# Kernel tuning notes

Hardware: AMD Instinct MI355X
Metric: run time of the kernel (lower is better)

## Reference

```python
import jax, jax.numpy as jnp
import numpy as np

HEADS = 8
DIM_HEAD = 64
SCALE = DIM_HEAD ** -0.5


def setup_inputs() -> dict:
    key = jax.random.key(0)
    ks = jax.random.split(key, 7)
    B, Nq, Nc = 4, 2048, 2048
    Dq, Dc = 1024, 768
    inner = HEADS * DIM_HEAD  # 512
    x = jax.random.normal(ks[0], (B, Nq, Dq), dtype=jnp.float32)
    context = jax.random.normal(ks[1], (B, Nc, Dc), dtype=jnp.float32)
    # Linear weights stored as (in, out) so y = x @ W, matching torch Linear math.
    Wq = jax.random.normal(ks[2], (Dq, inner), dtype=jnp.float32) * (Dq ** -0.5)
    Wk = jax.random.normal(ks[3], (Dc, inner), dtype=jnp.float32) * (Dc ** -0.5)
    Wv = jax.random.normal(ks[4], (Dc, inner), dtype=jnp.float32) * (Dc ** -0.5)
    Wo = jax.random.normal(ks[5], (inner, Dq), dtype=jnp.float32) * (inner ** -0.5)
    bo = jax.random.normal(ks[6], (Dq,), dtype=jnp.float32) * 0.01
    return {"x": x, "context": context, "Wq": Wq, "Wk": Wk, "Wv": Wv, "Wo": Wo, "bo": bo}


def reference(x, context, Wq, Wk, Wv, Wo, bo):
    B, Nq, _ = x.shape
    # projections -> [b, n, h, d]
    q = (x @ Wq).reshape(B, Nq, HEADS, DIM_HEAD)
    k = (context @ Wk).reshape(B, context.shape[1], HEADS, DIM_HEAD)
    v = (context @ Wv).reshape(B, context.shape[1], HEADS, DIM_HEAD)
    # scores [b, h, i, j]
    sim = jnp.einsum('bihd,bjhd->bhij', q, k) * SCALE
    attn = jax.nn.softmax(sim, axis=-1)
    out = jnp.einsum('bhij,bjhd->bihd', attn, v)  # [b, i, h, d]
    out = out.reshape(B, Nq, HEADS * DIM_HEAD)
    return out @ Wo + bo
```

## Files before the change

kernel.cpp:

```cpp
#include <hip/hip_runtime.h>
#include <hip/hip_bf16.h>


typedef __bf16 bf16_8 __attribute__((ext_vector_type(8)));
typedef __bf16 bf16_4 __attribute__((ext_vector_type(4)));
typedef float f32_4 __attribute__((ext_vector_type(4)));
typedef float f32_16 __attribute__((ext_vector_type(16)));
typedef int i32x2 __attribute__((ext_vector_type(2)));
typedef int i32x4 __attribute__((ext_vector_type(4)));

#define AS1 __attribute__((address_space(1)))
#define AS3 __attribute__((address_space(3)))

__device__ __forceinline__ void gld_lds16(const __bf16* g, __bf16* l) {
  __builtin_amdgcn_global_load_lds((AS1 unsigned int*)(void*)g,
                                   (AS3 unsigned int*)(void*)l, 16, 0, 0);
}

__device__ __forceinline__ void lds_fence() {
  __asm__ volatile("" ::: "memory");
  __builtin_amdgcn_s_waitcnt(0xC07F);
  __asm__ volatile("" ::: "memory");
}

__device__ __forceinline__ int cvt_pk(float lo, float hi) {
  int r;
  __asm__("v_cvt_pk_bf16_f32 %0, %1, %2" : "=v"(r) : "v"(lo), "v"(hi));
  return r;
}

__global__ __launch_bounds__(256) void prep(
    const float* __restrict__ x, const float* __restrict__ ctx,
    const float* __restrict__ Wq, const float* __restrict__ Wk,
    const float* __restrict__ Wv, const float* __restrict__ Wo,
    __bf16* __restrict__ xb, __bf16* __restrict__ ctxb,
    __bf16* __restrict__ WqT, __bf16* __restrict__ WkT,
    __bf16* __restrict__ WvT, __bf16* __restrict__ WoT) {
  int tb = blockIdx.x;
  if (tb >= 1792) {
    tb -= 1792;
    const float* src;
    __bf16* dst;
    size_t base;
    if (tb < 4096) { src = x; dst = xb; base = (size_t)tb * 2048; }
    else { src = ctx; dst = ctxb; base = (size_t)(tb - 4096) * 2048; }
    const size_t idx = base + threadIdx.x * 8;
    const f32_4 f0 = *(const f32_4*)(src + idx);
    const f32_4 f1 = *(const f32_4*)(src + idx + 4);
    bf16_8 v;
#pragma unroll
    for (int i = 0; i < 4; ++i) { v[i] = (__bf16)f0[i]; v[4 + i] = (__bf16)f1[i]; }
    *(bf16_8*)(dst + idx) = v;
    return;
  }
  __shared__ __bf16 t[32][33];
  const float* W; __bf16* Wt; int K, N;
  if (tb < 512)       { W = Wq; Wt = WqT; K = 1024; N = 512; }
  else if (tb < 896)  { tb -= 512;  W = Wk; Wt = WkT; K = 768; N = 512; }
  else if (tb < 1280) { tb -= 896;  W = Wv; Wt = WvT; K = 768; N = 512; }
  else                { tb -= 1280; W = Wo; Wt = WoT; K = 512; N = 1024; }
  const int nx = N >> 5;
  const int n0 = (tb % nx) * 32, k0 = (tb / nx) * 32;
  const int tx = threadIdx.x & 31, ty = threadIdx.x >> 5;
#pragma unroll
  for (int r = 0; r < 32; r += 8)
    t[ty + r][tx] = (__bf16)W[(size_t)(k0 + ty + r) * N + n0 + tx];
  __syncthreads();
#pragma unroll
  for (int r = 0; r < 32; r += 8)
    Wt[(size_t)(n0 + ty + r) * K + k0 + tx] = t[tx][ty + r];
}

__global__ __launch_bounds__(256, 2) void proj(
    const __bf16* __restrict__ xb, const __bf16* __restrict__ ctxb,
    const __bf16* __restrict__ WqT, const __bf16* __restrict__ WkvT,
    __bf16* __restrict__ Qb, __bf16* __restrict__ Kbuf,
    __bf16* __restrict__ Vtb) {
  __shared__ __align__(16) __bf16 As[2][128 * 64];
  __shared__ __align__(16) __bf16 Bs[2][128 * 64];
  int tb = blockIdx.x;
  const __bf16 *A, *Bt;
  int K, bm, bn, mode;
  if (tb < 256) {
    A = xb; Bt = WqT; K = 1024; mode = 0;
    bn = (tb & 3) << 7; bm = (tb >> 2) << 7;
  } else {
    tb -= 256;
    A = ctxb; Bt = WkvT; K = 768; mode = 1;
    bn = (tb & 7) << 7; bm = (tb >> 3) << 7;
  }
  const int tid = threadIdx.x;
  const int lane = tid & 63;
  const int wave = tid >> 6;
  const int wi = (wave >> 1) * 64;
  const int wn = (wave & 1) * 64;
  const int lrow = lane & 15;
  const int quad = lane >> 4;
  const int lkey = lrow & 7;
  const int srow = tid >> 3;
  const int scol = (tid & 7) * 8;
  const int swz = (((scol >> 3) ^ (srow & 7)) * 8);

  f32_4 acc[4][4];
#pragma unroll
  for (int i = 0; i < 4; ++i)
#pragma unroll
    for (int j = 0; j < 4; ++j)
#pragma unroll
      for (int r = 0; r < 4; ++r) acc[i][j][r] = 0.0f;

  auto stage = [&](int buf, int kt) {
#pragma unroll
    for (int r = 0; r < 4; ++r) {
      const int row = r * 32 + srow;
      gld_lds16(A + (size_t)(bm + row) * K + kt + swz, &As[buf][row * 64 + scol]);
    }
#pragma unroll
    for (int r = 0; r < 4; ++r) {
      const int row = r * 32 + srow;
      gld_lds16(Bt + (size_t)(bn + row) * K + kt + swz, &Bs[buf][row * 64 + scol]);
    }
  };

  stage(0, 0);
  const int nkt = K >> 6;
  for (int kti = 0; kti < nkt; ++kti) {
    __syncthreads();
    if (kti + 1 < nkt) stage((kti + 1) & 1, (kti + 1) * 64);
    const __bf16* Asb = As[kti & 1];
    const __bf16* Bsb = Bs[kti & 1];
#pragma unroll
    for (int ks = 0; ks < 2; ++ks) {
      bf16_8 af[4], bfv[4];
#pragma unroll
      for (int t = 0; t < 4; ++t)
        af[t] = *(const bf16_8*)(Asb + (wi + t * 16 + lrow) * 64 +
                                 (((ks * 4 + quad) ^ lkey) * 8));
#pragma unroll
      for (int t = 0; t < 4; ++t)
        bfv[t] = *(const bf16_8*)(Bsb + (wn + t * 16 + lrow) * 64 +
                                  (((ks * 4 + quad) ^ lkey) * 8));
#pragma unroll
      for (int it = 0; it < 4; ++it)
#pragma unroll
        for (int nt = 0; nt < 4; ++nt)
          acc[it][nt] = __builtin_amdgcn_mfma_f32_16x16x32_bf16(
              af[it], bfv[nt], acc[it][nt], 0, 0, 0);
    }
  }

#pragma unroll
  for (int nt = 0; nt < 4; ++nt) {
    const int c = bn + wn + nt * 16 + lrow;
    if (mode == 0) {
#pragma unroll
      for (int it = 0; it < 4; ++it) {
        const int rbase = bm + wi + it * 16 + quad * 4;
#pragma unroll
        for (int r = 0; r < 4; ++r)
          Qb[(size_t)(rbase + r) * 512 + c] = (__bf16)(acc[it][nt][r] * 0.125f);
      }
    } else if (c < 512) {
#pragma unroll
      for (int it = 0; it < 4; ++it) {
        const int rbase = bm + wi + it * 16 + quad * 4;
#pragma unroll
        for (int r = 0; r < 4; ++r)
          Kbuf[(size_t)(rbase + r) * 512 + c] = (__bf16)acc[it][nt][r];
      }
    } else {
      const int vcol = c - 512;
      const int bhh = ((bm >> 11) << 3) + (vcol >> 6);
      const int d = vcol & 63;
#pragma unroll
      for (int it = 0; it < 4; ++it) {
        const int jb = (bm & 2047) + wi + it * 16 + quad * 4;
        bf16_4 pk;
#pragma unroll
        for (int r = 0; r < 4; ++r) pk[r] = (__bf16)acc[it][nt][r];
        *(bf16_4*)&Vtb[((size_t)(bhh * 64 + d)) * 2048 + jb] = pk;
      }
    }
  }
}

__global__ __launch_bounds__(256, 3) void attn_fwd(const __bf16* __restrict__ Q,
                                                   const __bf16* __restrict__ Kb,
                                                   const __bf16* __restrict__ Vt,
                                                   __bf16* __restrict__ AO) {
  __shared__ __align__(16) __bf16 Ks[2][64 * 64];
  __shared__ __align__(16) __bf16 Vs[2][64 * 64];
  __shared__ __align__(16) float Ls[4][32];
  const int tid = threadIdx.x;
  const int lane = tid & 63;
  const int wave = tid >> 6;
  const int did = blockIdx.x;
  const int sid = did >> 3;
  const int bh = ((did & 7) << 2) + (sid & 3);
  const int ib = sid >> 2;
  const int b = bh >> 3, h = bh & 7;
  const int i0 = ib * 128 + wave * 32;
  const int li = lane & 31;
  const int hi = lane >> 5;
  const int key = li & 7;
  const size_t bq = (size_t)b * 2048;
  const int hc = h * 64;

  const int ssub = lane >> 3;
  const int sch = lane & 7;
  const int sswz = (sch ^ ssub) * 8;

  const __bf16* Kg = Kb + bq * 512 + hc;
  const __bf16* Vg = Vt + (size_t)bh * 64 * 2048;

  auto stage = [&](int buf, int j0) {
#pragma unroll
    for (int t = 0; t < 2; ++t) {
      const int rb = wave * 16 + t * 8;
      gld_lds16(Kg + (size_t)(j0 + rb + ssub) * 512 + sswz, &Ks[buf][rb * 64]);
      gld_lds16(Vg + (size_t)(rb + ssub) * 2048 + j0 + sswz, &Vs[buf][rb * 64]);
    }
  };

  bf16_8 aq[4];
#pragma unroll
  for (int ks = 0; ks < 4; ++ks)
    aq[ks] = *(const bf16_8*)(Q + (bq + i0 + li) * 512 + hc + ks * 16 + hi * 8);

  float psl = 0.0f;
  f32_16 oacc[2];
#pragma unroll
  for (int d = 0; d < 2; ++d)
#pragma unroll
    for (int r = 0; r < 16; ++r) oacc[d][r] = 0.0f;

  stage(0, 0);

  for (int jt = 0; jt < 32; ++jt) {
    __syncthreads();
    if (jt + 1 < 32) stage((jt + 1) & 1, (jt + 1) * 64);
    const __bf16* Ksb = Ks[jt & 1];
    const __bf16* Vsb = Vs[jt & 1];

    f32_16 sacc[2];
#pragma unroll
    for (int jb = 0; jb < 2; ++jb)
#pragma unroll
      for (int r = 0; r < 16; ++r) sacc[jb][r] = 0.0f;
    __builtin_amdgcn_s_setprio(1);
#pragma unroll
    for (int jb = 0; jb < 2; ++jb) {
#pragma unroll
      for (int ks = 0; ks < 4; ++ks) {
        const bf16_8 ak = *(const bf16_8*)(
            Ksb + (jb * 32 + li) * 64 + (((ks * 2 + hi) ^ key) * 8));
        sacc[jb] = __builtin_amdgcn_mfma_f32_32x32x16_bf16(
            ak, aq[ks], sacc[jb], 0, 0, 0);
      }
    }
    __builtin_amdgcn_s_setprio(0);

    int pw[4][4];
#pragma unroll
    for (int jb = 0; jb < 2; ++jb) {
      float p[16];
#pragma unroll
      for (int r = 0; r < 16; ++r) p[r] = __expf(sacc[jb][r]);
      float s0 = 0.0f, s1 = 0.0f;
#pragma unroll
      for (int r = 0; r < 8; ++r) { s0 += p[2 * r]; s1 += p[2 * r + 1]; }
      psl += s0 + s1;
      const int c01 = cvt_pk(p[0], p[1]),   c23 = cvt_pk(p[2], p[3]);
      const int c45 = cvt_pk(p[4], p[5]),   c67 = cvt_pk(p[6], p[7]);
      const int c89 = cvt_pk(p[8], p[9]),   cab = cvt_pk(p[10], p[11]);
      const int ccd = cvt_pk(p[12], p[13]), cef = cvt_pk(p[14], p[15]);
      const i32x2 r02 = __builtin_amdgcn_permlane32_swap(c01, c45, false, false);
      const i32x2 r13 = __builtin_amdgcn_permlane32_swap(c23, c67, false, false);
      const i32x2 r46 = __builtin_amdgcn_permlane32_swap(c89, ccd, false, false);
      const i32x2 r57 = __builtin_amdgcn_permlane32_swap(cab, cef, false, false);
      pw[jb * 2][0] = r02[0];     pw[jb * 2][1] = r13[0];
      pw[jb * 2][2] = r02[1];     pw[jb * 2][3] = r13[1];
      pw[jb * 2 + 1][0] = r46[0]; pw[jb * 2 + 1][1] = r57[0];
      pw[jb * 2 + 1][2] = r46[1]; pw[jb * 2 + 1][3] = r57[1];
    }

    __builtin_amdgcn_s_setprio(1);
#pragma unroll
    for (int ks2 = 0; ks2 < 4; ++ks2) {
      i32x4 w4;
      w4[0] = pw[ks2][0]; w4[1] = pw[ks2][1];
      w4[2] = pw[ks2][2]; w4[3] = pw[ks2][3];
      const bf16_8 ap = __builtin_bit_cast(bf16_8, w4);
#pragma unroll
      for (int dblk = 0; dblk < 2; ++dblk) {
        const bf16_8 bv = *(const bf16_8*)(
            Vsb + (dblk * 32 + li) * 64 + (((ks2 * 2 + hi) ^ key) * 8));
        oacc[dblk] = __builtin_amdgcn_mfma_f32_32x32x16_bf16(
            ap, bv, oacc[dblk], 0, 0, 0);
      }
    }
    __builtin_amdgcn_s_setprio(0);
  }

  const float tot = psl + __shfl_xor(psl, 32);
  const float inv = 1.0f / tot;
  if (lane < 32) Ls[wave][li] = inv;
  lds_fence();
  f32_4 ic[4];
#pragma unroll
  for (int g = 0; g < 4; ++g)
    ic[g] = *(const f32_4*)(&Ls[wave][8 * g + 4 * hi]);

#pragma unroll
  for (int dblk = 0; dblk < 2; ++dblk)
#pragma unroll
    for (int g = 0; g < 4; ++g)
#pragma unroll
      for (int r = 0; r < 4; ++r) {
        const size_t rg = bq + i0 + 8 * g + 4 * hi + r;
        AO[rg * 512 + hc + dblk * 32 + li] =
            (__bf16)(oacc[dblk][4 * g + r] * ic[g][r]);
      }
}

__global__ __launch_bounds__(256, 2) void gemm_out(const __bf16* __restrict__ A,
                                                   const __bf16* __restrict__ Bt,
                                                   float* __restrict__ C,
                                                   const float* __restrict__ bias) {
  __shared__ __align__(16) __bf16 As[2][128 * 64];
  __shared__ __align__(16) __bf16 Bs[2][128 * 64];
  const int K = 512, N = 1024;
  const int tid = threadIdx.x;
  const int lane = tid & 63;
  const int wave = tid >> 6;
  const int wi = (wave >> 1) * 64;
  const int wn = (wave & 1) * 64;
  const int bm = blockIdx.y * 128;
  const int bn = blockIdx.x * 128;
  const int lrow = lane & 15;
  const int quad = lane >> 4;
  const int lkey = lrow & 7;
  const int srow = tid >> 3;
  const int scol = (tid & 7) * 8;
  const int swz = (((scol >> 3) ^ (srow & 7)) * 8);

  f32_4 acc[4][4];
#pragma unroll
  for (int i = 0; i < 4; ++i)
#pragma unroll
    for (int j = 0; j < 4; ++j)
#pragma unroll
      for (int r = 0; r < 4; ++r) acc[i][j][r] = 0.0f;

  auto stage = [&](int buf, int kt) {
#pragma unroll
    for (int r = 0; r < 4; ++r) {
      const int row = r * 32 + srow;
      gld_lds16(A + (size_t)(bm + row) * K + kt + swz, &As[buf][row * 64 + scol]);
      gld_lds16(Bt + (size_t)(bn + row) * K + kt + swz, &Bs[buf][row * 64 + scol]);
    }
  };

  stage(0, 0);
  for (int kti = 0; kti < 8; ++kti) {
    __syncthreads();
    if (kti + 1 < 8) stage((kti + 1) & 1, (kti + 1) * 64);
    const __bf16* Asb = As[kti & 1];
    const __bf16* Bsb = Bs[kti & 1];
#pragma unroll
    for (int ks = 0; ks < 2; ++ks) {
      bf16_8 af[4], bfv[4];
#pragma unroll
      for (int t = 0; t < 4; ++t)
        af[t] = *(const bf16_8*)(Asb + (wi + t * 16 + lrow) * 64 +
                                 (((ks * 4 + quad) ^ lkey) * 8));
#pragma unroll
      for (int t = 0; t < 4; ++t)
        bfv[t] = *(const bf16_8*)(Bsb + (wn + t * 16 + lrow) * 64 +
                                  (((ks * 4 + quad) ^ lkey) * 8));
#pragma unroll
      for (int it = 0; it < 4; ++it)
#pragma unroll
        for (int nt = 0; nt < 4; ++nt)
          acc[it][nt] = __builtin_amdgcn_mfma_f32_16x16x32_bf16(
              af[it], bfv[nt], acc[it][nt], 0, 0, 0);
    }
  }

#pragma unroll
  for (int nt = 0; nt < 4; ++nt) {
    const int c = bn + wn + nt * 16 + lrow;
    const float bv = bias[c];
#pragma unroll
    for (int it = 0; it < 4; ++it) {
      const int rbase = bm + wi + it * 16 + quad * 4;
#pragma unroll
      for (int r = 0; r < 4; ++r)
        C[(size_t)(rbase + r) * N + c] = acc[it][nt][r] + bv;
    }
  }
}

extern "C" void kernel_launch(void* const* d_in, const int* in_sizes, int n_in,
                              void* d_out, int out_size, void* d_ws, size_t ws_size,
                              hipStream_t stream) {
  (void)in_sizes; (void)n_in; (void)out_size; (void)ws_size;
  const float* x   = (const float*)d_in[0];
  const float* ctx = (const float*)d_in[1];
  const float* Wq  = (const float*)d_in[2];
  const float* Wk  = (const float*)d_in[3];
  const float* Wv  = (const float*)d_in[4];
  const float* Wo  = (const float*)d_in[5];
  const float* bo  = (const float*)d_in[6];

  __bf16* ws = (__bf16*)d_ws;
  __bf16* WqT  = ws;
  __bf16* WkT  = WqT + 512 * 1024;
  __bf16* WvT  = WkT + 512 * 768;
  __bf16* WoT  = WvT + 512 * 768;
  __bf16* Qb   = WoT + 1024 * 512;
  __bf16* Kbuf = Qb + 8192 * 512;
  __bf16* Vtb  = Kbuf + 8192 * 512;
  __bf16* AOb  = Vtb + 8192 * 512;
  __bf16* xb   = AOb + 8192 * 512;
  __bf16* ctxb = xb + 8192 * 1024;

  prep<<<8960, 256, 0, stream>>>(x, ctx, Wq, Wk, Wv, Wo,
                                 xb, ctxb, WqT, WkT, WvT, WoT);

  proj<<<768, 256, 0, stream>>>(xb, ctxb, WqT, WkT, Qb, Kbuf, Vtb);

  attn_fwd<<<512, 256, 0, stream>>>(Qb, Kbuf, Vtb, AOb);

  gemm_out<<<dim3(8, 64), 256, 0, stream>>>(AOb, WoT, (float*)d_out, bo);
}
```

Before: 217.3 us.

## Split attention key range across two wave groups per block and merge in LDS

The attention kernel goes from 256 to 512 threads per block. The second group of four waves handles the second half of the key sequence, with separate double-buffered K/V staging. At the end, the second group writes its unnormalized output accumulators and row sums to LDS. The first group adds them, normalizes and stores the result. The aim is more waves in flight per CU and hidden load latency, at the cost of an extra LDS reduction, two more barriers and higher LDS use per block.

```diff
diff --git a/kernel.cpp b/kernel.cpp
--- a/kernel.cpp
+++ b/kernel.cpp
@@ -15,12 +15,6 @@
 __device__ __forceinline__ void gld_lds16(const __bf16* g, __bf16* l) {
   __builtin_amdgcn_global_load_lds((AS1 unsigned int*)(void*)g,
                                    (AS3 unsigned int*)(void*)l, 16, 0, 0);
-}
-
-__device__ __forceinline__ void lds_fence() {
-  __asm__ volatile("" ::: "memory");
-  __builtin_amdgcn_s_waitcnt(0xC07F);
-  __asm__ volatile("" ::: "memory");
 }
 
 __device__ __forceinline__ int cvt_pk(float lo, float hi) {
@@ -184,22 +178,23 @@
   }
 }
 
-__global__ __launch_bounds__(256, 3) void attn_fwd(const __bf16* __restrict__ Q,
+__global__ __launch_bounds__(512, 4) void attn_fwd(const __bf16* __restrict__ Q,
                                                    const __bf16* __restrict__ Kb,
                                                    const __bf16* __restrict__ Vt,
                                                    __bf16* __restrict__ AO) {
-  __shared__ __align__(16) __bf16 Ks[2][64 * 64];
-  __shared__ __align__(16) __bf16 Vs[2][64 * 64];
-  __shared__ __align__(16) float Ls[4][32];
+  __shared__ __align__(16) __bf16 KVs[4][2][64 * 64];
+  __shared__ __align__(16) float Ls[8][32];
   const int tid = threadIdx.x;
   const int lane = tid & 63;
   const int wave = tid >> 6;
+  const int wq = wave & 3;
+  const int jhalf = wave >> 2;
   const int did = blockIdx.x;
   const int sid = did >> 3;
   const int bh = ((did & 7) << 2) + (sid & 3);
   const int ib = sid >> 2;
   const int b = bh >> 3, h = bh & 7;
-  const int i0 = ib * 128 + wave * 32;
+  const int i0 = ib * 128 + wq * 32;
   const int li = lane & 31;
   const int hi = lane >> 5;
   const int key = li & 7;
@@ -212,13 +207,17 @@
 
   const __bf16* Kg = Kb + bq * 512 + hc;
   const __bf16* Vg = Vt + (size_t)bh * 64 * 2048;
+  __bf16* Ksl = &KVs[jhalf * 2 + 0][0][0];
+  __bf16* Vsl = &KVs[jhalf * 2 + 1][0][0];
 
   auto stage = [&](int buf, int j0) {
 #pragma unroll
     for (int t = 0; t < 2; ++t) {
-      const int rb = wave * 16 + t * 8;
-      gld_lds16(Kg + (size_t)(j0 + rb + ssub) * 512 + sswz, &Ks[buf][rb * 64]);
-      gld_lds16(Vg + (size_t)(rb + ssub) * 2048 + j0 + sswz, &Vs[buf][rb * 64]);
+      const int rb = wq * 16 + t * 8;
+      gld_lds16(Kg + (size_t)(j0 + rb + ssub) * 512 + sswz,
+                Ksl + buf * 4096 + rb * 64);
+      gld_lds16(Vg + (size_t)(rb + ssub) * 2048 + j0 + sswz,
+                Vsl + buf * 4096 + rb * 64);
     }
   };
 
@@ -234,13 +233,14 @@
 #pragma unroll
     for (int r = 0; r < 16; ++r) oacc[d][r] = 0.0f;
 
-  stage(0, 0);
-
-  for (int jt = 0; jt < 32; ++jt) {
+  const int jbase = jhalf * 1024;
+  stage(0, jbase);
+
+  for (int jt = 0; jt < 16; ++jt) {
     __syncthreads();
-    if (jt + 1 < 32) stage((jt + 1) & 1, (jt + 1) * 64);
-    const __bf16* Ksb = Ks[jt & 1];
-    const __bf16* Vsb = Vs[jt & 1];
+    if (jt + 1 < 16) stage((jt + 1) & 1, jbase + (jt + 1) * 64);
+    const __bf16* Ksb = Ksl + (jt & 1) * 4096;
+    const __bf16* Vsb = Vsl + (jt & 1) * 4096;
 
     f32_16 sacc[2];
 #pragma unroll
@@ -302,25 +302,45 @@
     __builtin_amdgcn_s_setprio(0);
   }
 
+  __syncthreads();
+  float* Cs = (float*)&KVs[0][0][0];
+
   const float tot = psl + __shfl_xor(psl, 32);
-  const float inv = 1.0f / tot;
-  if (lane < 32) Ls[wave][li] = inv;
-  lds_fence();
-  f32_4 ic[4];
-#pragma unroll
-  for (int g = 0; g < 4; ++g)
-    ic[g] = *(const f32_4*)(&Ls[wave][8 * g + 4 * hi]);
-
-#pragma unroll
-  for (int dblk = 0; dblk < 2; ++dblk)
-#pragma unroll
-    for (int g = 0; g < 4; ++g)
-#pragma unroll
-      for (int r = 0; r < 4; ++r) {
-        const size_t rg = bq + i0 + 8 * g + 4 * hi + r;
-        AO[rg * 512 + hc + dblk * 32 + li] =
-            (__bf16)(oacc[dblk][4 * g + r] * ic[g][r]);
-      }
+  if (lane < 32) Ls[wave][li] = tot;
+
+  if (jhalf == 1) {
+    float* Cw = Cs + wq * 2048;
+#pragma unroll
+    for (int dblk = 0; dblk < 2; ++dblk)
+#pragma unroll
+      for (int g = 0; g < 4; ++g)
+#pragma unroll
+        for (int r = 0; r < 4; ++r)
+          Cw[(8 * g + 4 * hi + r) * 64 + dblk * 32 + li] = oacc[dblk][4 * g + r];
+  }
+  __syncthreads();
+
+  if (jhalf == 0) {
+    const float* Cw = Cs + wq * 2048;
+    f32_4 s0[4], s1[4];
+#pragma unroll
+    for (int g = 0; g < 4; ++g) {
+      s0[g] = *(const f32_4*)(&Ls[wq][8 * g + 4 * hi]);
+      s1[g] = *(const f32_4*)(&Ls[wq + 4][8 * g + 4 * hi]);
+    }
+#pragma unroll
+    for (int dblk = 0; dblk < 2; ++dblk)
+#pragma unroll
+      for (int g = 0; g < 4; ++g)
+#pragma unroll
+        for (int r = 0; r < 4; ++r) {
+          const int rl = 8 * g + 4 * hi + r;
+          const float o = oacc[dblk][4 * g + r] + Cw[rl * 64 + dblk * 32 + li];
+          const float inv = 1.0f / (s0[g][r] + s1[g][r]);
+          const size_t rg = bq + i0 + rl;
+          AO[rg * 512 + hc + dblk * 32 + li] = (__bf16)(o * inv);
+        }
+  }
 }
 
 __global__ __launch_bounds__(256, 2) void gemm_out(const __bf16* __restrict__ A,
@@ -430,7 +450,7 @@
 
   proj<<<768, 256, 0, stream>>>(xb, ctxb, WqT, WkT, Qb, Kbuf, Vtb);
 
-  attn_fwd<<<512, 256, 0, stream>>>(Qb, Kbuf, Vtb, AOb);
+  attn_fwd<<<512, 512, 0, stream>>>(Qb, Kbuf, Vtb, AOb);
 
   gemm_out<<<dim3(8, 64), 256, 0, stream>>>(AOb, WoT, (float*)d_out, bo);
 }
```

Result: no change. 215.5 us (-0.8%).
